# Kernel optimization log

Hardware: AMD Instinct MI355X
Metric: run time of the kernel (lower is better)

Reference implementation:

```python
import jax, jax.numpy as jnp
import numpy as np

D = 8           # spatial size of conv feature map
K = 24          # conv channels
Q = 128         # question embedding size
IN_SIZE = 2 * (K + 2) + Q  # 180
HID = 256
OUT = 28


def _coords(d):
    # faithful to torch float-tensor arithmetic: a/d is float division
    a = jnp.arange(d * d, dtype=jnp.float32)
    cx = (a / d - d / 2) / (d / 2.0)
    cy = (a % d - d / 2) / (d / 2.0)
    return jnp.stack([cx, cy], axis=1)  # [d^2, 2]


def setup_inputs() -> dict:
    key = jax.random.key(0)
    ks = jax.random.split(key, 16)
    s = 0.05
    inp = {
        "x": jax.random.normal(ks[0], (64, K, D, D), dtype=jnp.float32),
        "qst": jax.random.normal(ks[1], (64, Q), dtype=jnp.float32),
        # g MLP (weights stored [in, out])
        "g1_w": jax.random.normal(ks[2], (IN_SIZE, HID), dtype=jnp.float32) * s,
        "g1_b": jnp.zeros((HID,), dtype=jnp.float32),
        "g2_w": jax.random.normal(ks[3], (HID, HID), dtype=jnp.float32) * s,
        "g2_b": jnp.zeros((HID,), dtype=jnp.float32),
        "g3_w": jax.random.normal(ks[4], (HID, HID), dtype=jnp.float32) * s,
        "g3_b": jnp.zeros((HID,), dtype=jnp.float32),
        "g4_w": jax.random.normal(ks[5], (HID, HID), dtype=jnp.float32) * s,
        "g4_b": jnp.zeros((HID,), dtype=jnp.float32),
        # f MLP
        "f1_w": jax.random.normal(ks[6], (HID, HID), dtype=jnp.float32) * s,
        "f1_b": jnp.zeros((HID,), dtype=jnp.float32),
        "f2_w": jax.random.normal(ks[7], (HID, HID), dtype=jnp.float32) * s,
        "f2_b": jnp.zeros((HID,), dtype=jnp.float32),
        "f3_w": jax.random.normal(ks[8], (HID, OUT), dtype=jnp.float32) * s,
        "f3_b": jnp.zeros((OUT,), dtype=jnp.float32),
    }
    return inp


def _forward(x, qst, g1_w, g1_b, g2_w, g2_b, g3_w, g3_b, g4_w, g4_b,
             f1_w, f1_b, f2_w, f2_b, f3_w, f3_b):
    b, k, d, _ = x.shape
    n = d * d  # 64 objects
    # [b, n, k] object features + 2 coord channels -> [b, n, 26]
    xf = jnp.transpose(x.reshape(b, k, n), (0, 2, 1))
    ct = jnp.broadcast_to(_coords(d)[None], (b, n, 2))
    xf = jnp.concatenate([xf, ct], axis=2)                      # [b, n, 26]
    obj = k + 2
    # x_i: varies along axis 2 (original torch layout); x_j varies along axis 1 and carries qst
    xi = jnp.broadcast_to(xf[:, None, :, :], (b, n, n, obj))
    xjq = jnp.concatenate(
        [xf, jnp.broadcast_to(qst[:, None, :], (b, n, qst.shape[1]))], axis=2)
    xj = jnp.broadcast_to(xjq[:, :, None, :], (b, n, n, obj + qst.shape[1]))
    pair = jnp.concatenate([xi, xj], axis=3)                    # [b, n, n, 180]
    # g MLP over all pairs
    h = jax.nn.relu(pair @ g1_w + g1_b)
    h = jax.nn.relu(h @ g2_w + g2_b)
    h = jax.nn.relu(h @ g3_w + g3_b)
    h = jax.nn.relu(h @ g4_w + g4_b)                            # [b, n, n, 256]
    xg = jnp.sum(h, axis=(1, 2))                                # sum over d^4 pairs
    # f MLP (dropout is identity in eval mode)
    xf_ = jax.nn.relu(xg @ f1_w + f1_b)
    xf_ = jax.nn.relu(xf_ @ f2_w + f2_b)
    logits = xf_ @ f3_w + f3_b
    return jax.nn.log_softmax(logits, axis=-1)


def reference(x, qst, g1_w, g1_b, g2_w, g2_b, g3_w, g3_b, g4_w, g4_b,
              f1_w, f1_b, f2_w, f2_b, f3_w, f3_b):
    return _forward(x, qst, g1_w, g1_b, g2_w, g2_b, g3_w, g3_b, g4_w, g4_b,
                    f1_w, f1_b, f2_w, f2_b, f3_w, f3_b)
```

## Files before the change

kernel.cpp:

```cpp
#include <hip/hip_runtime.h>

typedef __bf16 bf16_t;
typedef __bf16 bf16x8 __attribute__((ext_vector_type(8)));
typedef __bf16 bf16x4 __attribute__((ext_vector_type(4)));
typedef float  f32x4  __attribute__((ext_vector_type(4)));


__global__ __launch_bounds__(256) void rn_prep_kernel(
    const float* __restrict__ x, const float* __restrict__ qst,
    const float* __restrict__ g1w, const float* __restrict__ g1b,
    const float* __restrict__ g2w, const float* __restrict__ g3w,
    const float* __restrict__ g4w,
    float* __restrict__ A, float* __restrict__ C,
    bf16_t* __restrict__ Wt)
{
  __shared__ float T[64][65];
  int blk = blockIdx.x;
  int n   = threadIdx.x;
  if (blk < 256) {
    int b  = blk >> 2;
    int jg = (blk & 3) * 16;
    float accQ = g1b[n];
    const float* qb = qst + b * 128;
    #pragma unroll 8
    for (int qi = 0; qi < 128; ++qi)
      accQ += qb[qi] * g1w[(52 + qi) * 256 + n];

    float w24 = g1w[24 * 256 + n], w25 = g1w[25 * 256 + n];
    float w50 = g1w[50 * 256 + n], w51 = g1w[51 * 256 + n];
    float accA[16], accC[16];
    #pragma unroll
    for (int t = 0; t < 16; ++t) {
      int j = jg + t;
      float cx = ((float)j * 0.125f - 4.0f) * 0.25f;
      float cy = ((float)(j & 7) - 4.0f) * 0.25f;
      accA[t] = cx * w24 + cy * w25;
      accC[t] = accQ + cx * w50 + cy * w51;
    }
    for (int c = 0; c < 24; ++c) {
      float wa = g1w[c * 256 + n];
      float wc = g1w[(26 + c) * 256 + n];
      const float* xc = x + (b * 24 + c) * 64 + jg;
      #pragma unroll
      for (int t = 0; t < 16; ++t) {
        float xv = xc[t];
        accA[t] += xv * wa;
        accC[t] += xv * wc;
      }
    }
    #pragma unroll
    for (int t = 0; t < 16; ++t) {
      A[(b * 64 + jg + t) * 256 + n] = accA[t];
      C[(b * 64 + jg + t) * 256 + n] = accC[t];
    }
  } else {
    int t   = blk - 256;
    int mat = t >> 4;
    int tl  = t & 15;
    int kt  = (tl & 3) * 64;
    int nt_ = (tl >> 2) * 64;
    const float* W = (mat == 0) ? g2w : (mat == 1 ? g3w : g4w);
    int lane = n & 63, w = n >> 6;
    #pragma unroll
    for (int it = 0; it < 16; ++it) {
      int kl = w * 16 + it;
      T[kl][lane] = W[(kt + kl) * 256 + nt_ + lane];
    }
    __syncthreads();
    #pragma unroll
    for (int it = 0; it < 16; ++it) {
      int nl  = w * 16 + it;
      int no  = nt_ + nl;
      int k   = kt + lane;
      int tile = no >> 4, rr = no & 15;
      int ksI  = k >> 5,  qI = (k >> 3) & 3, e = k & 7;
      int idx  = ((tile * 8 + ksI) * 64 + qI * 16 + rr) * 8 + e;
      Wt[mat * 65536 + idx] = (bf16_t)T[lane][nl];
    }
  }
}

__global__ __launch_bounds__(256, 1) void rn_main_kernel(
    const float* __restrict__ A, const float* __restrict__ C,
    const bf16_t* __restrict__ Wt,
    const float* __restrict__ g2b, const float* __restrict__ g3b,
    const float* __restrict__ g4b,
    float* __restrict__ part)
{
  __shared__ bf16_t h0[16384];
  __shared__ bf16_t h1[16384];

  int tid  = threadIdx.x;
  int bx0  = blockIdx.x;
  int bx   = (bx0 & 7) * 256 + (bx0 >> 3);
  int b    = bx >> 5;
  int ip   = bx & 31;
  int lane = tid & 63;
  int wave = tid >> 6;
  int r    = lane & 15;
  int q    = lane >> 4;

  {
    const float* Ab = A + (size_t)b * 64 * 256;
    const float* Cr = C + ((size_t)b * 64 + ip * 2) * 256;
    int j = wave * 16 + r;
    #pragma unroll
    for (int it = 0; it < 8; ++it) {
      int k0 = it * 32 + q * 8;
      const float4 a0  = *(const float4*)(Ab + j * 256 + k0);
      const float4 a1  = *(const float4*)(Ab + j * 256 + k0 + 4);
      const float4 c00 = *(const float4*)(Cr + k0);
      const float4 c01 = *(const float4*)(Cr + k0 + 4);
      const float4 c10 = *(const float4*)(Cr + 256 + k0);
      const float4 c11 = *(const float4*)(Cr + 256 + k0 + 4);
      bf16x8 v0, v1;
      v0[0] = (bf16_t)fmaxf(a0.x + c00.x, 0.f);
      v0[1] = (bf16_t)fmaxf(a0.y + c00.y, 0.f);
      v0[2] = (bf16_t)fmaxf(a0.z + c00.z, 0.f);
      v0[3] = (bf16_t)fmaxf(a0.w + c00.w, 0.f);
      v0[4] = (bf16_t)fmaxf(a1.x + c01.x, 0.f);
      v0[5] = (bf16_t)fmaxf(a1.y + c01.y, 0.f);
      v0[6] = (bf16_t)fmaxf(a1.z + c01.z, 0.f);
      v0[7] = (bf16_t)fmaxf(a1.w + c01.w, 0.f);
      v1[0] = (bf16_t)fmaxf(a0.x + c10.x, 0.f);
      v1[1] = (bf16_t)fmaxf(a0.y + c10.y, 0.f);
      v1[2] = (bf16_t)fmaxf(a0.z + c10.z, 0.f);
      v1[3] = (bf16_t)fmaxf(a0.w + c10.w, 0.f);
      v1[4] = (bf16_t)fmaxf(a1.x + c11.x, 0.f);
      v1[5] = (bf16_t)fmaxf(a1.y + c11.y, 0.f);
      v1[6] = (bf16_t)fmaxf(a1.z + c11.z, 0.f);
      v1[7] = (bf16_t)fmaxf(a1.w + c11.w, 0.f);
      int off = ((wave * 8 + it) * 64 + lane) * 8;
      *(bf16x8*)&h0[off] = v0;
      *(bf16x8*)&h1[off] = v1;
    }
  }

  for (int L = 0; L < 3; ++L) {
    const bf16_t* Wl = Wt + L * 65536 + wave * 16384;
    bf16x8 wreg[4][8];
    #pragma unroll
    for (int nt = 0; nt < 4; ++nt)
      #pragma unroll
      for (int ks = 0; ks < 8; ++ks)
        wreg[nt][ks] = *(const bf16x8*)&Wl[((nt * 8 + ks) * 64 + lane) * 8];

    const float* bias = (L == 0) ? g2b : (L == 1) ? g3b : g4b;

    __syncthreads();

    f32x4 acc[4][8];
    #pragma unroll
    for (int nt = 0; nt < 4; ++nt)
      #pragma unroll
      for (int mt = 0; mt < 8; ++mt)
        #pragma unroll
        for (int e = 0; e < 4; ++e) acc[nt][mt][e] = 0.f;

    #pragma unroll
    for (int ks = 0; ks < 8; ++ks) {
      bf16x8 hf[8];
      #pragma unroll
      for (int mt = 0; mt < 8; ++mt) {
        const bf16_t* hb = (mt < 4) ? h0 : h1;
        hf[mt] = *(const bf16x8*)&hb[(((mt & 3) * 8 + ks) * 64 + lane) * 8];
      }
      #pragma unroll
      for (int nt = 0; nt < 4; ++nt)
        #pragma unroll
        for (int mt = 0; mt < 8; ++mt)
          acc[nt][mt] = __builtin_amdgcn_mfma_f32_16x16x32_bf16(
              wreg[nt][ks], hf[mt], acc[nt][mt], 0, 0, 0);
    }

    __syncthreads();

    if (L < 2) {
      #pragma unroll
      for (int nt = 0; nt < 4; ++nt) {
        int k0  = wave * 64 + nt * 16 + q * 4;
        float4 bv = *(const float4*)&bias[k0];
        int ks_ = k0 >> 5, rem = k0 & 31;
        int qp  = rem >> 3, e0 = rem & 7;
        #pragma unroll
        for (int mt = 0; mt < 8; ++mt) {
          bf16_t* hb = (mt < 4) ? h0 : h1;
          bf16x4 v;
          v[0] = (bf16_t)fmaxf(acc[nt][mt][0] + bv.x, 0.f);
          v[1] = (bf16_t)fmaxf(acc[nt][mt][1] + bv.y, 0.f);
          v[2] = (bf16_t)fmaxf(acc[nt][mt][2] + bv.z, 0.f);
          v[3] = (bf16_t)fmaxf(acc[nt][mt][3] + bv.w, 0.f);
          int off = (((mt & 3) * 8 + ks_) * 64 + qp * 16 + r) * 8 + e0;
          *(bf16x4*)&hb[off] = v;
        }
      }
    } else {
      #pragma unroll
      for (int nt = 0; nt < 4; ++nt) {
        int k0 = wave * 64 + nt * 16 + q * 4;
        float4 bv = *(const float4*)&bias[k0];
        float p0 = 0.f, p1 = 0.f, p2 = 0.f, p3 = 0.f;
        #pragma unroll
        for (int mt = 0; mt < 8; ++mt) {
          p0 += fmaxf(acc[nt][mt][0] + bv.x, 0.f);
          p1 += fmaxf(acc[nt][mt][1] + bv.y, 0.f);
          p2 += fmaxf(acc[nt][mt][2] + bv.z, 0.f);
          p3 += fmaxf(acc[nt][mt][3] + bv.w, 0.f);
        }
        #pragma unroll
        for (int d = 1; d < 16; d <<= 1) {
          p0 += __shfl_xor(p0, d, 64);
          p1 += __shfl_xor(p1, d, 64);
          p2 += __shfl_xor(p2, d, 64);
          p3 += __shfl_xor(p3, d, 64);
        }
        if (r == 0) {
          float4 pv = make_float4(p0, p1, p2, p3);
          *(float4*)&part[(size_t)bx * 256 + k0] = pv;
        }
      }
    }
  }
}

__global__ __launch_bounds__(256) void rn_f_kernel(
    const float* __restrict__ part,
    const float* __restrict__ f1w, const float* __restrict__ f1b,
    const float* __restrict__ f2w, const float* __restrict__ f2b,
    const float* __restrict__ f3w, const float* __restrict__ f3b,
    float* __restrict__ out)
{
  __shared__ float xs[256], t1[256], t2[256], lg[28], lse[1];
  int b = blockIdx.x, tid = threadIdx.x;
  float s = 0.f;
  const float* pb = part + (size_t)b * 32 * 256;
  #pragma unroll 8
  for (int i = 0; i < 32; ++i) s += pb[i * 256 + tid];
  xs[tid] = s;
  __syncthreads();
  float acc = f1b[tid];
  for (int k = 0; k < 256; ++k) acc += xs[k] * f1w[k * 256 + tid];
  t1[tid] = fmaxf(acc, 0.f);
  __syncthreads();
  acc = f2b[tid];
  for (int k = 0; k < 256; ++k) acc += t1[k] * f2w[k * 256 + tid];
  t2[tid] = fmaxf(acc, 0.f);
  __syncthreads();
  if (tid < 28) {
    float a2 = f3b[tid];
    for (int k = 0; k < 256; ++k) a2 += t2[k] * f3w[k * 28 + tid];
    lg[tid] = a2;
  }
  __syncthreads();
  if (tid == 0) {
    float m = lg[0];
    for (int j = 1; j < 28; ++j) m = fmaxf(m, lg[j]);
    float se = 0.f;
    for (int j = 0; j < 28; ++j) se += expf(lg[j] - m);
    lse[0] = m + logf(se);
  }
  __syncthreads();
  if (tid < 28) out[b * 28 + tid] = lg[tid] - lse[0];
}

extern "C" void kernel_launch(void* const* d_in, const int* in_sizes, int n_in,
                              void* d_out, int out_size, void* d_ws, size_t ws_size,
                              hipStream_t stream) {
  (void)in_sizes; (void)n_in; (void)out_size; (void)ws_size;
  const float* x   = (const float*)d_in[0];
  const float* qst = (const float*)d_in[1];
  const float* g1w = (const float*)d_in[2];
  const float* g1b = (const float*)d_in[3];
  const float* g2w = (const float*)d_in[4];
  const float* g2b = (const float*)d_in[5];
  const float* g3w = (const float*)d_in[6];
  const float* g3b = (const float*)d_in[7];
  const float* g4w = (const float*)d_in[8];
  const float* g4b = (const float*)d_in[9];
  const float* f1w = (const float*)d_in[10];
  const float* f1b = (const float*)d_in[11];
  const float* f2w = (const float*)d_in[12];
  const float* f2b = (const float*)d_in[13];
  const float* f3w = (const float*)d_in[14];
  const float* f3b = (const float*)d_in[15];
  float* out = (float*)d_out;

  float*  A    = (float*)d_ws;
  float*  C    = A + 4096 * 256;
  bf16_t* Wt   = (bf16_t*)(C + 4096 * 256);
  float*  part = (float*)((char*)Wt + 3 * 65536 * sizeof(bf16_t));

  rn_prep_kernel<<<256 + 48, 256, 0, stream>>>(
      x, qst, g1w, g1b, g2w, g3w, g4w, A, C, Wt);
  rn_main_kernel<<<2048, 256, 0, stream>>>(A, C, Wt, g2b, g3b, g4b, part);
  rn_f_kernel<<<64, 256, 0, stream>>>(part, f1w, f1b, f2w, f2b, f3w, f3b, out);
}
```

Before: 251.3 us.

## Ping-pong LDS activations, stream weights per k-step, pre-swizzle A layout

```diff
diff --git a/kernel.cpp b/kernel.cpp
--- a/kernel.cpp
+++ b/kernel.cpp
@@ -11,7 +11,7 @@
     const float* __restrict__ g1w, const float* __restrict__ g1b,
     const float* __restrict__ g2w, const float* __restrict__ g3w,
     const float* __restrict__ g4w,
-    float* __restrict__ A, float* __restrict__ C,
+    float* __restrict__ Ap, float* __restrict__ C,
     bf16_t* __restrict__ Wt)
 {
   __shared__ float T[64][65];
@@ -48,9 +48,12 @@
         accC[t] += xv * wc;
       }
     }
+    int jt = blk & 3;
+    int itA = n >> 5, qA = (n >> 3) & 3, eA = n & 7;
+    int baseA = b * 16384 + (jt * 8 + itA) * 512 + qA * 128 + eA;
     #pragma unroll
     for (int t = 0; t < 16; ++t) {
-      A[(b * 64 + jg + t) * 256 + n] = accA[t];
+      Ap[baseA + t * 8] = accA[t];
       C[(b * 64 + jg + t) * 256 + n] = accC[t];
     }
   } else {
@@ -81,14 +84,14 @@
 }
 
 __global__ __launch_bounds__(256, 1) void rn_main_kernel(
-    const float* __restrict__ A, const float* __restrict__ C,
+    const float* __restrict__ Ap, const float* __restrict__ C,
     const bf16_t* __restrict__ Wt,
     const float* __restrict__ g2b, const float* __restrict__ g3b,
     const float* __restrict__ g4b,
     float* __restrict__ part)
 {
-  __shared__ bf16_t h0[16384];
-  __shared__ bf16_t h1[16384];
+  __shared__ bf16_t hA[32768];
+  __shared__ bf16_t hB[32768];
 
   int tid  = threadIdx.x;
   int bx0  = blockIdx.x;
@@ -101,14 +104,13 @@
   int q    = lane >> 4;
 
   {
-    const float* Ab = A + (size_t)b * 64 * 256;
-    const float* Cr = C + ((size_t)b * 64 + ip * 2) * 256;
-    int j = wave * 16 + r;
+    const float* Apb = Ap + (size_t)b * 16384 + wave * 4096;
+    const float* Cr  = C + ((size_t)b * 64 + ip * 2) * 256;
     #pragma unroll
     for (int it = 0; it < 8; ++it) {
       int k0 = it * 32 + q * 8;
-      const float4 a0  = *(const float4*)(Ab + j * 256 + k0);
-      const float4 a1  = *(const float4*)(Ab + j * 256 + k0 + 4);
+      const float4 a0  = *(const float4*)(Apb + it * 512 + lane * 8);
+      const float4 a1  = *(const float4*)(Apb + it * 512 + lane * 8 + 4);
       const float4 c00 = *(const float4*)(Cr + k0);
       const float4 c01 = *(const float4*)(Cr + k0 + 4);
       const float4 c10 = *(const float4*)(Cr + 256 + k0);
@@ -130,50 +132,45 @@
       v1[5] = (bf16_t)fmaxf(a1.y + c11.y, 0.f);
       v1[6] = (bf16_t)fmaxf(a1.z + c11.z, 0.f);
       v1[7] = (bf16_t)fmaxf(a1.w + c11.w, 0.f);
-      int off = ((wave * 8 + it) * 64 + lane) * 8;
-      *(bf16x8*)&h0[off] = v0;
-      *(bf16x8*)&h1[off] = v1;
-    }
-  }
-
+      *(bf16x8*)&hA[((wave * 8 + it) * 64 + lane) * 8] = v0;
+      *(bf16x8*)&hA[(((4 + wave) * 8 + it) * 64 + lane) * 8] = v1;
+    }
+  }
+  __syncthreads();
+
+  #pragma unroll
   for (int L = 0; L < 3; ++L) {
-    const bf16_t* Wl = Wt + L * 65536 + wave * 16384;
-    bf16x8 wreg[4][8];
+    const bf16_t* hs = (L == 1) ? hB : hA;
+    bf16_t*       hd = (L == 0) ? hB : hA;
+    const bf16_t* Wl   = Wt + L * 65536 + wave * 16384;
+    const float*  bias = (L == 0) ? g2b : (L == 1) ? g3b : g4b;
+
+    f32x4 acc[4][8];
     #pragma unroll
     for (int nt = 0; nt < 4; ++nt)
       #pragma unroll
-      for (int ks = 0; ks < 8; ++ks)
-        wreg[nt][ks] = *(const bf16x8*)&Wl[((nt * 8 + ks) * 64 + lane) * 8];
-
-    const float* bias = (L == 0) ? g2b : (L == 1) ? g3b : g4b;
-
-    __syncthreads();
-
-    f32x4 acc[4][8];
-    #pragma unroll
-    for (int nt = 0; nt < 4; ++nt)
-      #pragma unroll
       for (int mt = 0; mt < 8; ++mt)
         #pragma unroll
         for (int e = 0; e < 4; ++e) acc[nt][mt][e] = 0.f;
 
     #pragma unroll
     for (int ks = 0; ks < 8; ++ks) {
-      bf16x8 hf[8];
-      #pragma unroll
-      for (int mt = 0; mt < 8; ++mt) {
-        const bf16_t* hb = (mt < 4) ? h0 : h1;
-        hf[mt] = *(const bf16x8*)&hb[(((mt & 3) * 8 + ks) * 64 + lane) * 8];
-      }
+      bf16x8 wf[4], hf[8];
+      #pragma unroll
+      for (int nt = 0; nt < 4; ++nt)
+        wf[nt] = *(const bf16x8*)&Wl[((nt * 8 + ks) * 64 + lane) * 8];
+      #pragma unroll
+      for (int mt = 0; mt < 8; ++mt)
+        hf[mt] = *(const bf16x8*)&hs[((mt * 8 + ks) * 64 + lane) * 8];
+      __builtin_amdgcn_s_setprio(1);
       #pragma unroll
       for (int nt = 0; nt < 4; ++nt)
         #pragma unroll
         for (int mt = 0; mt < 8; ++mt)
           acc[nt][mt] = __builtin_amdgcn_mfma_f32_16x16x32_bf16(
-              wreg[nt][ks], hf[mt], acc[nt][mt], 0, 0, 0);
-    }
-
-    __syncthreads();
+              wf[nt], hf[mt], acc[nt][mt], 0, 0, 0);
+      __builtin_amdgcn_s_setprio(0);
+    }
 
     if (L < 2) {
       #pragma unroll
@@ -184,16 +181,16 @@
         int qp  = rem >> 3, e0 = rem & 7;
         #pragma unroll
         for (int mt = 0; mt < 8; ++mt) {
-          bf16_t* hb = (mt < 4) ? h0 : h1;
           bf16x4 v;
           v[0] = (bf16_t)fmaxf(acc[nt][mt][0] + bv.x, 0.f);
           v[1] = (bf16_t)fmaxf(acc[nt][mt][1] + bv.y, 0.f);
           v[2] = (bf16_t)fmaxf(acc[nt][mt][2] + bv.z, 0.f);
           v[3] = (bf16_t)fmaxf(acc[nt][mt][3] + bv.w, 0.f);
-          int off = (((mt & 3) * 8 + ks_) * 64 + qp * 16 + r) * 8 + e0;
-          *(bf16x4*)&hb[off] = v;
+          int off = ((mt * 8 + ks_) * 64 + qp * 16 + r) * 8 + e0;
+          *(bf16x4*)&hd[off] = v;
         }
       }
+      __syncthreads();
     } else {
       #pragma unroll
       for (int nt = 0; nt < 4; ++nt) {
@@ -285,13 +282,13 @@
   const float* f3b = (const float*)d_in[15];
   float* out = (float*)d_out;
 
-  float*  A    = (float*)d_ws;
-  float*  C    = A + 4096 * 256;
+  float*  Ap   = (float*)d_ws;
+  float*  C    = Ap + 4096 * 256;
   bf16_t* Wt   = (bf16_t*)(C + 4096 * 256);
   float*  part = (float*)((char*)Wt + 3 * 65536 * sizeof(bf16_t));
 
   rn_prep_kernel<<<256 + 48, 256, 0, stream>>>(
-      x, qst, g1w, g1b, g2w, g3w, g4w, A, C, Wt);
-  rn_main_kernel<<<2048, 256, 0, stream>>>(A, C, Wt, g2b, g3b, g4b, part);
+      x, qst, g1w, g1b, g2w, g3w, g4w, Ap, C, Wt);
+  rn_main_kernel<<<2048, 256, 0, stream>>>(Ap, C, Wt, g2b, g3b, g4b, part);
   rn_f_kernel<<<64, 256, 0, stream>>>(part, f1w, f1b, f2w, f2b, f3w, f3b, out);
 }
```

After: 240.1 us. 1.05x faster.
